# Kernel tuning notes

Measured on AMD Instinct MI355X. Metric: run time of the kernel, lower is better.

Reference implementation:

```python
import jax, jax.numpy as jnp
import numpy as np

TS = (32, 32, 32)          # tensor_size per dim
NC = 32 * 32 * 32          # total grid cells
HEADS = 4


def setup_inputs() -> dict:
    key = jax.random.key(0)
    k1, k2, k3 = jax.random.split(key, 3)
    B, H, V, N = 4, HEADS, 8, 16384
    local_coordinate = jax.random.uniform(k1, (B, H, V, N), dtype=jnp.float32)
    flattened_index = jax.random.randint(k2, (B, H, V, N), 0, NC, dtype=jnp.int64)
    features = jax.random.normal(k3, (B, 128, N), dtype=jnp.float32)
    return {"local_coordinate": local_coordinate,
            "flattened_index": flattened_index,
            "features": features}


def reference(local_coordinate, flattened_index, features):
    # local_coordinate: [B, H, V, N], flattened_index: [B, H, V, N] int64
    # features: [B, H*fd, N]
    B, H, V, N = local_coordinate.shape
    fd = features.shape[1] // H
    feats = features.reshape(B, H, fd, N)
    # outer-product splat: [B, H, fd, V, N]
    pre_splat = feats[:, :, :, None, :] * local_coordinate[:, :, None, :, :]
    src = pre_splat.reshape(B, H, fd, V * N)
    idx = flattened_index.reshape(B, H, V * N)

    def scat(s, i):
        # s: [fd, V*N], i: [V*N]; out initialized to zeros like torch scatter_max with zero out
        return jnp.zeros((fd, NC), dtype=s.dtype).at[:, i].max(s)

    z = jax.vmap(jax.vmap(scat))(src, idx)  # [B, H, fd, NC]
    return z.reshape(B, H * fd, *TS)
```

## Files before the change

kernel.cpp:

```cpp
#include <hip/hip_runtime.h>
#include <hip/hip_bf16.h>

constexpr int B  = 4;
constexpr int H  = 4;
constexpr int V  = 8;
constexpr int N  = 16384;
constexpr int FD = 32;
constexpr int NC = 32768;
constexpr int BH = B * H;
constexpr int VN = V * N;
constexpr int NPAIR = BH * VN;

constexpr int CB   = 1024;
constexpr int CAPB = 208;
constexpr int TP   = 8192;

constexpr size_t OFF_BCNT   = 0;
constexpr size_t OFF_SLOTS  = OFF_BCNT  + (size_t)BH * CB;
constexpr size_t OFF_FEATST = OFF_SLOTS + (size_t)BH * CB * CAPB;

__device__ __forceinline__ unsigned short f2bf(float v) {
    unsigned int u = __float_as_uint(v);
    return (unsigned short)((u + 0x7FFFu + ((u >> 16) & 1u)) >> 16);
}

__global__ __launch_bounds__(256)
void k_transpose(const float* __restrict__ feats,
                 unsigned short* __restrict__ featsT) {
    __shared__ float tile[32][33];
    int bh = blockIdx.x;
    int n0 = blockIdx.y * 32;
    int tx = threadIdx.x;
    int ty = threadIdx.y;
#pragma unroll
    for (int fr = 0; fr < 4; ++fr) {
        int f = ty + fr * 8;
        tile[f][tx] = feats[((size_t)bh * FD + f) * N + n0 + tx];
    }
    __syncthreads();
#pragma unroll
    for (int nr = 0; nr < 4; ++nr) {
        int n = ty + nr * 8;
        featsT[((size_t)bh * N + n0 + n) * FD + tx] = f2bf(tile[tx][n]);
    }
}

__global__ __launch_bounds__(1024)
void k_scatter_ms(const int* __restrict__ idx, const float* __restrict__ lc,
                  int* __restrict__ bcnt, unsigned int* __restrict__ slots) {
    __shared__ __align__(16) unsigned int kkey[TP];
    __shared__ __align__(8)  unsigned short cbuf[TP];
    __shared__ int cnt[CB];
    __shared__ int base[CB];
    const int tid = threadIdx.x;
    const size_t t0 = (size_t)blockIdx.x * TP;
    const int bh = (int)(t0 >> 17);

    cnt[tid] = 0;
    __syncthreads();

    const int4*   idx4 = (const int4*)(idx + t0);
    const float4* lc4  = (const float4*)(lc + t0);
    const int nb = (int)(t0 & (N - 1));
#pragma unroll
    for (int r = 0; r < 2; ++r) {
        int i = tid + r * 1024;
        int4   c4 = idx4[i];
        float4 l4 = lc4[i];
        unsigned int n0 = (unsigned int)(nb + i * 4);
        unsigned int q0 = (unsigned int)(l4.x * 8192.0f);
        unsigned int q1 = (unsigned int)(l4.y * 8192.0f);
        unsigned int q2 = (unsigned int)(l4.z * 8192.0f);
        unsigned int q3 = (unsigned int)(l4.w * 8192.0f);
        uint4 kk;
        kk.x = ((unsigned int)(c4.x & 31) << 27) | (q0 << 14) | n0;
        kk.y = ((unsigned int)(c4.y & 31) << 27) | (q1 << 14) | (n0 + 1);
        kk.z = ((unsigned int)(c4.z & 31) << 27) | (q2 << 14) | (n0 + 2);
        kk.w = ((unsigned int)(c4.w & 31) << 27) | (q3 << 14) | (n0 + 3);
        ((uint4*)kkey)[i] = kk;
        ushort4 cc;
        cc.x = (unsigned short)(c4.x >> 5);
        cc.y = (unsigned short)(c4.y >> 5);
        cc.z = (unsigned short)(c4.z >> 5);
        cc.w = (unsigned short)(c4.w >> 5);
        ((ushort4*)cbuf)[i] = cc;
        atomicAdd(&cnt[c4.x >> 5], 1);
        atomicAdd(&cnt[c4.y >> 5], 1);
        atomicAdd(&cnt[c4.z >> 5], 1);
        atomicAdd(&cnt[c4.w >> 5], 1);
    }
    __syncthreads();

    {
        int c = cnt[tid];
        base[tid] = (c > 0) ? atomicAdd(&bcnt[bh * CB + tid], c) : 0;
        cnt[tid] = 0;
    }
    __syncthreads();

#pragma unroll
    for (int r = 0; r < 8; ++r) {
        int i = tid + r * 1024;
        int cb = cbuf[i];
        int p  = atomicAdd(&cnt[cb], 1);
        int pos = base[cb] + p;
        if (pos < CAPB)
            slots[((size_t)bh * CB + cb) * CAPB + pos] = kkey[i];
    }
}

__global__ __launch_bounds__(256)
void k_compute(const int* __restrict__ bcnt, const unsigned int* __restrict__ slots,
               const unsigned short* __restrict__ featsT, float* __restrict__ out) {
    __shared__ unsigned int acc[32][33];
    __shared__ unsigned int kbuf[CAPB];
    const int tid = threadIdx.x;
    const int bh  = blockIdx.x >> 10;
    const int cb  = blockIdx.x & (CB - 1);

    int cnt = bcnt[bh * CB + cb];
    if (cnt > CAPB) cnt = CAPB;
    const unsigned int* row = slots + ((size_t)bh * CB + cb) * CAPB;
    if (tid < cnt) kbuf[tid] = row[tid];
    for (int i = tid; i < 32 * 33; i += 256) ((unsigned int*)acc)[i] = 0u;
    __syncthreads();

    const int g = tid >> 5;
    const int f = tid & 31;
    const unsigned short* fT = featsT + (size_t)bh * N * FD;
    const int last = cnt - 1;

    for (int r0 = 8 * g; r0 < cnt; r0 += 64) {
        unsigned int k[8];
        float fv[8];
#pragma unroll
        for (int j = 0; j < 8; ++j)
            k[j] = kbuf[min(r0 + j, last)];
#pragma unroll
        for (int j = 0; j < 8; ++j) {
            int off = (int)((k[j] & 16383u) << 5) | f;
            fv[j] = __uint_as_float((unsigned int)fT[off] << 16);
        }
#pragma unroll
        for (int j = 0; j < 8; ++j) {
            float coord = ((float)((k[j] >> 14) & 8191u) + 0.5f) * (1.0f / 8192.0f);
            float val = fmaxf(coord * fv[j], 0.0f);
            atomicMax(&acc[k[j] >> 27][f], __float_as_uint(val));
        }
    }
    __syncthreads();

    int cell = tid & 31;
    int c0   = cb * 32;
#pragma unroll
    for (int i = 0; i < 4; ++i) {
        int ff = (tid >> 5) + i * 8;
        out[((size_t)(bh * FD + ff)) * NC + c0 + cell] =
            __uint_as_float(acc[cell][ff]);
    }
}

extern "C" void kernel_launch(void* const* d_in, const int* in_sizes, int n_in,
                              void* d_out, int out_size, void* d_ws, size_t ws_size,
                              hipStream_t stream) {
    const float* lc    = (const float*)d_in[0];
    const int*   idx   = (const int*)  d_in[1];
    const float* feats = (const float*)d_in[2];
    float* out = (float*)d_out;

    int*            bcnt   = (int*)d_ws + OFF_BCNT;
    unsigned int*   slots  = (unsigned int*)d_ws + OFF_SLOTS;
    unsigned short* featsT = (unsigned short*)((unsigned int*)d_ws + OFF_FEATST);

    hipMemsetAsync(bcnt, 0, (size_t)BH * CB * sizeof(int), stream);

    k_transpose<<<dim3(BH, N / 32), dim3(32, 8), 0, stream>>>(feats, featsT);
    k_scatter_ms<<<NPAIR / TP, 1024, 0, stream>>>(idx, lc, bcnt, slots);
    k_compute<<<BH * CB, 256, 0, stream>>>(bcnt, slots, featsT, out);
}
```

Before: 151.7 us.

## Merge transpose and scatter into one launch with locally bucket-sorted keys

```diff
diff --git a/kernel.cpp b/kernel.cpp
--- a/kernel.cpp
+++ b/kernel.cpp
@@ -14,6 +14,8 @@
 constexpr int CB   = 1024;
 constexpr int CAPB = 208;
 constexpr int TP   = 8192;
+constexpr int SB   = NPAIR / TP;
+constexpr int TB   = BH * (N / 128);
 
 constexpr size_t OFF_BCNT   = 0;
 constexpr size_t OFF_SLOTS  = OFF_BCNT  + (size_t)BH * CB;
@@ -24,88 +26,104 @@
     return (unsigned short)((u + 0x7FFFu + ((u >> 16) & 1u)) >> 16);
 }
 
-__global__ __launch_bounds__(256)
-void k_transpose(const float* __restrict__ feats,
-                 unsigned short* __restrict__ featsT) {
-    __shared__ float tile[32][33];
-    int bh = blockIdx.x;
-    int n0 = blockIdx.y * 32;
-    int tx = threadIdx.x;
-    int ty = threadIdx.y;
+__global__ __launch_bounds__(1024)
+void k_prep(const int* __restrict__ idx, const float* __restrict__ lc,
+            const float* __restrict__ feats, int* __restrict__ bcnt,
+            unsigned int* __restrict__ slots, unsigned short* __restrict__ featsT) {
+    __shared__ __align__(16) unsigned char smem[61440];
+    const int tid = threadIdx.x;
+
+    if (blockIdx.x < SB) {
+        unsigned int*   skey   = (unsigned int*)smem;
+        unsigned short* scb    = (unsigned short*)(smem + 32768);
+        int*            s      = (int*)(smem + 49152);
+        int*            cursor = (int*)(smem + 53248);
+        int*            rbase  = (int*)(smem + 57344);
+
+        const size_t t0 = (size_t)blockIdx.x * TP;
+        const int bh = (int)(t0 >> 17);
+
+        s[tid] = 0;
+        __syncthreads();
+
+        const int4* idx4 = (const int4*)(idx + t0);
+        int4 c4a[2];
 #pragma unroll
-    for (int fr = 0; fr < 4; ++fr) {
-        int f = ty + fr * 8;
-        tile[f][tx] = feats[((size_t)bh * FD + f) * N + n0 + tx];
-    }
-    __syncthreads();
+        for (int r = 0; r < 2; ++r) {
+            int4 c4 = idx4[tid + r * 1024];
+            c4a[r] = c4;
+            atomicAdd(&s[c4.x >> 5], 1);
+            atomicAdd(&s[c4.y >> 5], 1);
+            atomicAdd(&s[c4.z >> 5], 1);
+            atomicAdd(&s[c4.w >> 5], 1);
+        }
+        __syncthreads();
+        const int myc = s[tid];
+
+        for (int off = 1; off < 1024; off <<= 1) {
+            int v = (tid >= off) ? s[tid - off] : 0;
+            __syncthreads();
+            s[tid] += v;
+            __syncthreads();
+        }
+        const int scanstart = s[tid] - myc;
+        __syncthreads();
+        s[tid]      = scanstart;
+        cursor[tid] = scanstart;
+        rbase[tid]  = (myc > 0) ? atomicAdd(&bcnt[bh * CB + tid], myc) : 0;
+        __syncthreads();
+
+        const float4* lc4 = (const float4*)(lc + t0);
+        const unsigned int nb = (unsigned int)(t0 & (N - 1));
 #pragma unroll
-    for (int nr = 0; nr < 4; ++nr) {
-        int n = ty + nr * 8;
-        featsT[((size_t)bh * N + n0 + n) * FD + tx] = f2bf(tile[tx][n]);
-    }
-}
-
-__global__ __launch_bounds__(1024)
-void k_scatter_ms(const int* __restrict__ idx, const float* __restrict__ lc,
-                  int* __restrict__ bcnt, unsigned int* __restrict__ slots) {
-    __shared__ __align__(16) unsigned int kkey[TP];
-    __shared__ __align__(8)  unsigned short cbuf[TP];
-    __shared__ int cnt[CB];
-    __shared__ int base[CB];
-    const int tid = threadIdx.x;
-    const size_t t0 = (size_t)blockIdx.x * TP;
-    const int bh = (int)(t0 >> 17);
-
-    cnt[tid] = 0;
-    __syncthreads();
-
-    const int4*   idx4 = (const int4*)(idx + t0);
-    const float4* lc4  = (const float4*)(lc + t0);
-    const int nb = (int)(t0 & (N - 1));
+        for (int r = 0; r < 2; ++r) {
+            int i = tid + r * 1024;
+            int4   c4 = c4a[r];
+            float4 l4 = lc4[i];
+            unsigned int n0 = nb + (unsigned int)(i * 4);
+            int cx[4] = {c4.x, c4.y, c4.z, c4.w};
+            float lx[4] = {l4.x, l4.y, l4.z, l4.w};
 #pragma unroll
-    for (int r = 0; r < 2; ++r) {
-        int i = tid + r * 1024;
-        int4   c4 = idx4[i];
-        float4 l4 = lc4[i];
-        unsigned int n0 = (unsigned int)(nb + i * 4);
-        unsigned int q0 = (unsigned int)(l4.x * 8192.0f);
-        unsigned int q1 = (unsigned int)(l4.y * 8192.0f);
-        unsigned int q2 = (unsigned int)(l4.z * 8192.0f);
-        unsigned int q3 = (unsigned int)(l4.w * 8192.0f);
-        uint4 kk;
-        kk.x = ((unsigned int)(c4.x & 31) << 27) | (q0 << 14) | n0;
-        kk.y = ((unsigned int)(c4.y & 31) << 27) | (q1 << 14) | (n0 + 1);
-        kk.z = ((unsigned int)(c4.z & 31) << 27) | (q2 << 14) | (n0 + 2);
-        kk.w = ((unsigned int)(c4.w & 31) << 27) | (q3 << 14) | (n0 + 3);
-        ((uint4*)kkey)[i] = kk;
-        ushort4 cc;
-        cc.x = (unsigned short)(c4.x >> 5);
-        cc.y = (unsigned short)(c4.y >> 5);
-        cc.z = (unsigned short)(c4.z >> 5);
-        cc.w = (unsigned short)(c4.w >> 5);
-        ((ushort4*)cbuf)[i] = cc;
-        atomicAdd(&cnt[c4.x >> 5], 1);
-        atomicAdd(&cnt[c4.y >> 5], 1);
-        atomicAdd(&cnt[c4.z >> 5], 1);
-        atomicAdd(&cnt[c4.w >> 5], 1);
-    }
-    __syncthreads();
-
-    {
-        int c = cnt[tid];
-        base[tid] = (c > 0) ? atomicAdd(&bcnt[bh * CB + tid], c) : 0;
-        cnt[tid] = 0;
-    }
-    __syncthreads();
+            for (int e = 0; e < 4; ++e) {
+                unsigned int q = (unsigned int)(lx[e] * 8192.0f);
+                unsigned int key = ((unsigned int)(cx[e] & 31) << 27)
+                                 | (q << 14) | (n0 + e);
+                int cb = cx[e] >> 5;
+                int pos = atomicAdd(&cursor[cb], 1);
+                skey[pos] = key;
+                scb[pos]  = (unsigned short)cb;
+            }
+        }
+        __syncthreads();
 
 #pragma unroll
-    for (int r = 0; r < 8; ++r) {
-        int i = tid + r * 1024;
-        int cb = cbuf[i];
-        int p  = atomicAdd(&cnt[cb], 1);
-        int pos = base[cb] + p;
-        if (pos < CAPB)
-            slots[((size_t)bh * CB + cb) * CAPB + pos] = kkey[i];
+        for (int r = 0; r < 8; ++r) {
+            int j  = tid + r * 1024;
+            int cb = scb[j];
+            int gpos = rbase[cb] + (j - s[cb]);
+            if (gpos < CAPB)
+                slots[((size_t)bh * CB + cb) * CAPB + gpos] = skey[j];
+        }
+    } else {
+        float (*tile)[32][33] = (float (*)[32][33])smem;
+        int bi  = blockIdx.x - SB;
+        int bh  = bi >> 7;
+        int n0  = (bi & 127) * 128;
+        int sub = tid >> 8;
+        int tx  = tid & 31;
+        int ty  = (tid >> 5) & 7;
+        int nb  = n0 + sub * 32;
+#pragma unroll
+        for (int fr = 0; fr < 4; ++fr) {
+            int f = ty + fr * 8;
+            tile[sub][f][tx] = feats[((size_t)bh * FD + f) * N + nb + tx];
+        }
+        __syncthreads();
+#pragma unroll
+        for (int nr = 0; nr < 4; ++nr) {
+            int n = ty + nr * 8;
+            featsT[((size_t)bh * N + nb + n) * FD + tx] = f2bf(tile[sub][tx][n]);
+        }
     }
 }
 
@@ -155,8 +173,8 @@
 #pragma unroll
     for (int i = 0; i < 4; ++i) {
         int ff = (tid >> 5) + i * 8;
-        out[((size_t)(bh * FD + ff)) * NC + c0 + cell] =
-            __uint_as_float(acc[cell][ff]);
+        __builtin_nontemporal_store(__uint_as_float(acc[cell][ff]),
+            &out[((size_t)(bh * FD + ff)) * NC + c0 + cell]);
     }
 }
 
@@ -174,7 +192,6 @@
 
     hipMemsetAsync(bcnt, 0, (size_t)BH * CB * sizeof(int), stream);
 
-    k_transpose<<<dim3(BH, N / 32), dim3(32, 8), 0, stream>>>(feats, featsT);
-    k_scatter_ms<<<NPAIR / TP, 1024, 0, stream>>>(idx, lc, bcnt, slots);
+    k_prep<<<SB + TB, 1024, 0, stream>>>(idx, lc, feats, bcnt, slots, featsT);
     k_compute<<<BH * CB, 256, 0, stream>>>(bcnt, slots, featsT, out);
 }
```

Result: faster. 138.6 us (-8.6%).
